# Optimization experiments

Measured on AMD Instinct MI355X. Metric: run time of the kernel, lower is better.

## Reference

```python
import jax, jax.numpy as jnp
import numpy as np

D = 64       # hidden_dim
ED = 16      # edge_dim
N = 50000
E = 400000
T = 2
STEP = 0.5   # euler fixed step over t in [0,1] -> 2 steps
EPS = 1e-5

def setup_inputs() -> dict:
    key = jax.random.key(0)
    ks = jax.random.split(key, 14)
    def lin(k, fi, fo):
        return jax.random.normal(k, (fi, fo), jnp.float32) / np.sqrt(fi)
    return {
        'h_seq': jax.random.normal(ks[0], (T, N, D), jnp.float32),
        'edge_attr': jax.random.normal(ks[1], (T, E, ED), jnp.float32),
        # msg_net: MLP(2D+ED -> D -> D), 2 layers with ReLU
        'W1': lin(ks[2], 2 * D + ED, D), 'b1': jnp.zeros((D,), jnp.float32),
        'W2': lin(ks[3], D, D),          'b2': jnp.zeros((D,), jnp.float32),
        # dynamics_net: Linear(2D,D) -> LayerNorm -> SiLU -> Linear(D,D) -> Tanh
        'Wd1': lin(ks[4], 2 * D, D), 'bd1': jnp.zeros((D,), jnp.float32),
        'ln_g': jnp.ones((D,), jnp.float32), 'ln_b': jnp.zeros((D,), jnp.float32),
        'Wd2': lin(ks[5], D, D), 'bd2': jnp.zeros((D,), jnp.float32),
        'edge_index': jax.random.randint(ks[6], (T, 2, E), 0, N, jnp.int32),
    }

def _ode_func(h, row, col, ea, W1, b1, W2, b2, Wd1, bd1, ln_g, ln_b, Wd2, bd2):
    # identity transport: Q_uv @ h_v == h_v
    h_transported = h[col]                              # [E, D]
    msg_in = jnp.concatenate([h[row], h_transported, ea], axis=-1)  # [E, 2D+ED]
    msg = jax.nn.relu(msg_in @ W1 + b1) @ W2 + b2       # [E, D]
    agg = jax.ops.segment_sum(msg, row, num_segments=h.shape[0])    # [N, D]
    x = jnp.concatenate([h, agg], axis=-1) @ Wd1 + bd1  # [N, D]
    mu = x.mean(-1, keepdims=True)
    var = x.var(-1, keepdims=True)
    x = (x - mu) * jax.lax.rsqrt(var + EPS) * ln_g + ln_b
    x = jax.nn.silu(x) @ Wd2 + bd2
    return jnp.tanh(x)

def reference(h_seq, edge_attr, W1, b1, W2, b2, Wd1, bd1, ln_g, ln_b, Wd2, bd2, edge_index):
    params = (W1, b1, W2, b2, Wd1, bd1, ln_g, ln_b, Wd2, bd2)
    n_steps = int(round(1.0 / STEP))
    h_prev = h_seq[0]
    disagreements = []
    for t in range(T):
        row, col = edge_index[t, 0], edge_index[t, 1]
        ea = edge_attr[t]
        h = h_prev + h_seq[t]                           # h_fused
        for _ in range(n_steps):                        # fixed-step Euler
            h = h + STEP * _ode_func(h, row, col, ea, *params)
        diff = h[row] - h[col]                          # Q=I -> h_u - h_v
        disagreements.append(jnp.minimum((diff * diff).sum(-1), 1e4))
        h_prev = h
    return h_prev, jnp.stack(disagreements)             # h_final [N,D], D [T,E]
```

## Files before the change

kernel.cpp:

```cpp
#include <hip/hip_runtime.h>

#define NN 50000
#define EE 400000
#define NT64 6250
#define EGRID 1250
#define NBLK 782
#define SBLK 49

typedef __bf16 bf16x8 __attribute__((ext_vector_type(8)));
typedef float f32x4 __attribute__((ext_vector_type(4)));

static __device__ __forceinline__ ushort f2bf(float f) {
    union { float f; unsigned int i; } x; x.f = f;
    unsigned int r = x.i + 0x7fffu + ((x.i >> 16) & 1u);
    return (ushort)(r >> 16);
}
static __device__ __forceinline__ float bf2f(ushort u) {
    union { unsigned int i; float f; } x; x.i = ((unsigned int)u) << 16; return x.f;
}
static __device__ __forceinline__ unsigned pack2(float lo, float hi) {
    return (unsigned)f2bf(lo) | ((unsigned)f2bf(hi) << 16);
}
static __device__ __forceinline__ float fast_tanh(float x) {
    float e = __expf(2.f * x);
    return 1.f - 2.f / (e + 1.f);
}
static __device__ __forceinline__ bf16x8 pk8(float4 f0, float4 f1) {
    union { uint4 u; bf16x8 v; } z;
    z.u = make_uint4(pack2(f0.x, f0.y), pack2(f0.z, f0.w),
                     pack2(f1.x, f1.y), pack2(f1.z, f1.w));
    return z.v;
}
static __device__ __forceinline__ bf16x8 zero8() {
    union { uint4 u; bf16x8 v; } z;
    z.u = make_uint4(0u, 0u, 0u, 0u);
    return z.v;
}

__global__ __launch_bounds__(256) void prep_edge_k(
    const float* __restrict__ W1, const float* __restrict__ W2,
    const float* __restrict__ b1, const float* __restrict__ b2,
    ushort* __restrict__ B1P, ushort* __restrict__ B2P,
    float* __restrict__ b1f, float* __restrict__ b2f)
{
    int idx = blockIdx.x * 256 + threadIdx.x;
    if (idx < 10240) {
        int j = idx & 7, n = (idx >> 3) & 63, qk = idx >> 9;
        int kc = qk >> 2, quad = qk & 3;
        int k = kc * 32 + quad * 8 + j;
        B1P[idx] = (k < 144) ? f2bf(W1[k * 64 + n]) : (ushort)0;
    }
    if (idx < 4096) {
        int j = idx & 7, n = (idx >> 3) & 63, qk = idx >> 9;
        int kc = qk >> 2, quad = qk & 3;
        int k = kc * 32 + quad * 8 + j;
        B2P[idx] = f2bf(W2[k * 64 + n]);
    }
    if (idx < 64) { b1f[idx] = b1[idx]; b2f[idx] = b2[idx]; }
}

__global__ __launch_bounds__(256) void prep_node_k(
    const float* __restrict__ Wd1, const float* __restrict__ Wd2,
    const float* __restrict__ bd1, const float* __restrict__ lng,
    const float* __restrict__ lnb, const float* __restrict__ bd2,
    ushort* __restrict__ Wd1P, ushort* __restrict__ Wd2P,
    float* __restrict__ bd1f, float* __restrict__ lngf,
    float* __restrict__ lnbf, float* __restrict__ bd2f)
{
    int idx = blockIdx.x * 256 + threadIdx.x;
    if (idx < 8192) {
        int j = idx & 7, n = (idx >> 3) & 63, qk = idx >> 9;
        int kc = qk >> 2, quad = qk & 3;
        int k = kc * 32 + quad * 8 + j;
        Wd1P[idx] = f2bf(Wd1[k * 64 + n]);
    }
    if (idx < 4096) {
        int j = idx & 7, n = (idx >> 3) & 63, qk = idx >> 9;
        int kc = qk >> 2, quad = qk & 3;
        int k = kc * 32 + quad * 8 + j;
        Wd2P[idx] = f2bf(Wd2[k * 64 + n]);
    }
    if (idx < 64) {
        bd1f[idx] = bd1[idx]; lngf[idx] = lng[idx];
        lnbf[idx] = lnb[idx]; bd2f[idx] = bd2[idx];
    }
}

__global__ __launch_bounds__(256) void state_k(
    float* __restrict__ h, ushort* __restrict__ hb,
    const float* __restrict__ hseq_t, int mode)
{
    int i = blockIdx.x * 256 + threadIdx.x;
    float v = hseq_t[i];
    float r = (mode == 0) ? (2.f * v) : (h[i] + v);
    h[i] = r; hb[i] = f2bf(r);
}

__global__ __launch_bounds__(256) void zero_k(int* __restrict__ p, int n) {
    int i = blockIdx.x * 256 + threadIdx.x;
    if (i < n) p[i] = 0;
}
__global__ __launch_bounds__(256) void zero_f(float* __restrict__ p) {
    int i = blockIdx.x * 256 + threadIdx.x;
    p[i] = 0.f;
}
__global__ __launch_bounds__(256) void hist_k(const int* __restrict__ rows, int* __restrict__ counts) {
    int e = blockIdx.x * 256 + threadIdx.x;
    if (e < EE) atomicAdd(&counts[rows[e]], 1);
}

__global__ __launch_bounds__(256) void scanA_k(
    const int* __restrict__ counts, int* __restrict__ offsets, int* __restrict__ bsum)
{
    __shared__ int wsum[4];
    int tid = threadIdx.x, lane = tid & 63, w = tid >> 6;
    int i4 = blockIdx.x * 1024 + tid * 4;
    int4 v = make_int4(0, 0, 0, 0);
    if (i4 + 3 < NN) v = *(const int4*)(counts + i4);
    else {
        if (i4 < NN) v.x = counts[i4];
        if (i4 + 1 < NN) v.y = counts[i4 + 1];
        if (i4 + 2 < NN) v.z = counts[i4 + 2];
    }
    int s = v.x + v.y + v.z + v.w;
    int x = s;
    for (int off = 1; off < 64; off <<= 1) {
        int y = __shfl_up(x, off);
        if (lane >= off) x += y;
    }
    if (lane == 63) wsum[w] = x;
    __syncthreads();
    int wpre = 0;
    for (int j = 0; j < w; j++) wpre += wsum[j];
    int excl = wpre + x - s;
    int e0 = excl, e1 = e0 + v.x, e2 = e1 + v.y, e3 = e2 + v.z;
    if (i4 + 3 < NN) *(int4*)(offsets + i4) = make_int4(e0, e1, e2, e3);
    else {
        if (i4 < NN) offsets[i4] = e0;
        if (i4 + 1 < NN) offsets[i4 + 1] = e1;
        if (i4 + 2 < NN) offsets[i4 + 2] = e2;
    }
    if (tid == 255) bsum[blockIdx.x] = wpre + x;
}
__global__ __launch_bounds__(64) void scanB_k(const int* __restrict__ bsum, int* __restrict__ bpre) {
    int lane = threadIdx.x;
    int v = (lane < SBLK) ? bsum[lane] : 0;
    int x = v;
    for (int off = 1; off < 64; off <<= 1) {
        int y = __shfl_up(x, off);
        if (lane >= off) x += y;
    }
    if (lane < SBLK) bpre[lane] = x - v;
}
__global__ __launch_bounds__(256) void scanC_k(
    int* __restrict__ offsets, int* __restrict__ cursor, const int* __restrict__ bpre)
{
    int i = blockIdx.x * 256 + threadIdx.x;
    if (i < NN) {
        int o = offsets[i] + bpre[i >> 10];
        offsets[i] = o; cursor[i] = o;
    }
    if (i == 0) offsets[NN] = EE;
}

__global__ __launch_bounds__(256) void fill_k(
    const int* __restrict__ rows, const int* __restrict__ cols,
    const float* __restrict__ ea, int* __restrict__ cursor,
    int* __restrict__ rsort, int* __restrict__ csort, ushort* __restrict__ eab)
{
    int e = blockIdx.x * 256 + threadIdx.x;
    if (e < EE) {
        int r = rows[e];
        int p = atomicAdd(&cursor[r], 1);
        if ((unsigned)p < (unsigned)EE) {
            rsort[p] = r; csort[p] = cols[e];
            const float* sp = ea + (size_t)e * 16;
            float4 f0 = ((const float4*)sp)[0], f1 = ((const float4*)sp)[1];
            float4 f2 = ((const float4*)sp)[2], f3 = ((const float4*)sp)[3];
            uint4* dp = (uint4*)(eab + (size_t)p * 16);
            dp[0] = make_uint4(pack2(f0.x, f0.y), pack2(f0.z, f0.w),
                               pack2(f1.x, f1.y), pack2(f1.z, f1.w));
            dp[1] = make_uint4(pack2(f2.x, f2.y), pack2(f2.z, f2.w),
                               pack2(f3.x, f3.y), pack2(f3.z, f3.w));
        }
    }
}

template<int MODE>
__global__ __launch_bounds__(256, 5) void edge_k(
    const ushort* __restrict__ hb,
    const int* __restrict__ ridx, const int* __restrict__ cidx,
    const ushort* __restrict__ eab, const float* __restrict__ eaf,
    const ushort* __restrict__ B1P, const ushort* __restrict__ B2P,
    const float* __restrict__ b1f, const float* __restrict__ b2f,
    ushort* __restrict__ msg, float* __restrict__ agg)
{
    __shared__ __attribute__((aligned(16))) ushort sB1[10240];
    __shared__ __attribute__((aligned(16))) ushort sH[64 * 72];

    int tid = threadIdx.x;
    int lane = tid & 63, wave = tid >> 6;
    int m = lane & 15, quad = lane >> 4;

    for (int i = tid; i < 10240 / 8; i += 256) ((uint4*)sB1)[i] = ((const uint4*)B1P)[i];
    bf16x8 b2r[2][4];
    for (int kc = 0; kc < 2; kc++)
        for (int nt = 0; nt < 4; nt++)
            b2r[kc][nt] = *(const bf16x8*)(B2P + ((kc * 4 + quad) * 64 + nt * 16 + m) * 8);
    float b1v[4], b2v[4];
    for (int nt = 0; nt < 4; nt++) { b1v[nt] = b1f[nt * 16 + m]; b2v[nt] = b2f[nt * 16 + m]; }
    __syncthreads();

    ushort* sHw = sH + wave * 1152;
    int sl = wave * 16 + m;

    int spf = blockIdx.x * 64 + sl;
    int r_n = ridx[spf], c_n = cidx[spf];

    for (int t = blockIdx.x; t < NT64; t += EGRID) {
        int s = t * 64 + sl;
        int r = r_n, c = c_n;

        bf16x8 a[5];
        a[0] = *(const bf16x8*)(hb + (size_t)r * 64 + quad * 8);
        a[1] = *(const bf16x8*)(hb + (size_t)r * 64 + 32 + quad * 8);
        a[2] = *(const bf16x8*)(hb + (size_t)c * 64 + quad * 8);
        a[3] = *(const bf16x8*)(hb + (size_t)c * 64 + 32 + quad * 8);
        a[4] = zero8();
        if (MODE == 0) {
            if (quad < 2) a[4] = *(const bf16x8*)(eab + (size_t)s * 16 + quad * 8);
        } else {
            if (quad < 2) {
                const float* sp = eaf + (size_t)s * 16 + quad * 8;
                float4 f0 = ((const float4*)sp)[0], f1 = ((const float4*)sp)[1];
                a[4] = pk8(f0, f1);
            }
        }

        int tn = t + EGRID; if (tn >= NT64) tn = t;
        int sn = tn * 64 + sl;
        r_n = ridx[sn]; c_n = cidx[sn];

        f32x4 acc[4];
        #pragma unroll
        for (int nt = 0; nt < 4; nt++) acc[nt] = (f32x4){0.f, 0.f, 0.f, 0.f};
        #pragma unroll
        for (int kc = 0; kc < 5; kc++) {
            #pragma unroll
            for (int nt = 0; nt < 4; nt++) {
                bf16x8 b = *(const bf16x8*)(sB1 + ((kc * 4 + quad) * 64 + nt * 16 + m) * 8);
                acc[nt] = __builtin_amdgcn_mfma_f32_16x16x32_bf16(a[kc], b, acc[nt], 0, 0, 0);
            }
        }

        __builtin_amdgcn_wave_barrier();
        #pragma unroll
        for (int nt = 0; nt < 4; nt++) {
            int colid = nt * 16 + m;
            float bb = b1v[nt];
            #pragma unroll
            for (int rr = 0; rr < 4; rr++) {
                float v = acc[nt][rr] + bb;
                v = v > 0.f ? v : 0.f;
                sHw[(quad * 4 + rr) * 72 + colid] = f2bf(v);
            }
        }
        __builtin_amdgcn_wave_barrier();

        f32x4 acc2[4];
        #pragma unroll
        for (int nt = 0; nt < 4; nt++) acc2[nt] = (f32x4){0.f, 0.f, 0.f, 0.f};
        #pragma unroll
        for (int kc = 0; kc < 2; kc++) {
            bf16x8 av = *(const bf16x8*)(sHw + m * 72 + kc * 32 + quad * 8);
            #pragma unroll
            for (int nt = 0; nt < 4; nt++) {
                acc2[nt] = __builtin_amdgcn_mfma_f32_16x16x32_bf16(av, b2r[kc][nt], acc2[nt], 0, 0, 0);
            }
        }

        int rr4[4];
        if (MODE == 1) {
            #pragma unroll
            for (int rr = 0; rr < 4; rr++) rr4[rr] = ridx[t * 64 + wave * 16 + quad * 4 + rr];
        }
        #pragma unroll
        for (int nt = 0; nt < 4; nt++) {
            int colid = nt * 16 + m;
            float bb = b2v[nt];
            #pragma unroll
            for (int rr = 0; rr < 4; rr++) {
                float v = acc2[nt][rr] + bb;
                int so = t * 64 + wave * 16 + quad * 4 + rr;
                if (MODE == 0) {
                    msg[(size_t)so * 64 + colid] = f2bf(v);
                } else {
                    atomicAdd(&agg[(size_t)rr4[rr] * 64 + colid], v);
                }
            }
        }
    }
}

__global__ __launch_bounds__(256) void agg_k(
    const ushort* __restrict__ msg, const int* __restrict__ offsets,
    float* __restrict__ agg)
{
    int gw = (blockIdx.x * 256 + threadIdx.x) >> 6;
    int lane = threadIdx.x & 63;
    int beg = offsets[gw], end = offsets[gw + 1];
    beg = beg < 0 ? 0 : beg;
    end = end > EE ? EE : end;
    float a = 0.f;
    int i = beg;
    for (; i + 4 <= end; i += 4) {
        a += bf2f(msg[(size_t)i * 64 + lane]);
        a += bf2f(msg[(size_t)(i + 1) * 64 + lane]);
        a += bf2f(msg[(size_t)(i + 2) * 64 + lane]);
        a += bf2f(msg[(size_t)(i + 3) * 64 + lane]);
    }
    for (; i < end; i++) a += bf2f(msg[(size_t)i * 64 + lane]);
    agg[(size_t)gw * 64 + lane] = a;
}

__global__ __launch_bounds__(256, 4) void node_k(
    float* __restrict__ h, ushort* __restrict__ hbm,
    const float* __restrict__ agg,
    const ushort* __restrict__ Wd1P, const ushort* __restrict__ Wd2P,
    const float* __restrict__ bd1f, const float* __restrict__ lngf,
    const float* __restrict__ lnbf, const float* __restrict__ bd2f)
{
    __shared__ __attribute__((aligned(16))) ushort sB1[8192];
    __shared__ __attribute__((aligned(16))) ushort sB2[4096];
    __shared__ __attribute__((aligned(16))) ushort sX[64 * 72];
    int tid = threadIdx.x;
    int lane = tid & 63, wave = tid >> 6;
    int m = lane & 15, quad = lane >> 4;
    int nbase = blockIdx.x * 64;

    for (int i = tid; i < 8192 / 8; i += 256) ((uint4*)sB1)[i] = ((const uint4*)Wd1P)[i];
    for (int i = tid; i < 4096 / 8; i += 256) ((uint4*)sB2)[i] = ((const uint4*)Wd2P)[i];
    float gA[4], bA[4], d1[4], d2[4];
    for (int nt = 0; nt < 4; nt++) {
        int f = nt * 16 + m;
        d1[nt] = bd1f[f]; gA[nt] = lngf[f]; bA[nt] = lnbf[f]; d2[nt] = bd2f[f];
    }
    __syncthreads();

    int n = nbase + wave * 16 + m;
    if (n > NN - 1) n = NN - 1;
    bf16x8 A[4];
    A[0] = *(const bf16x8*)(hbm + (size_t)n * 64 + quad * 8);
    A[1] = *(const bf16x8*)(hbm + (size_t)n * 64 + 32 + quad * 8);
    {
        const float* ap = agg + (size_t)n * 64 + quad * 8;
        A[2] = pk8(((const float4*)ap)[0], ((const float4*)ap)[1]);
        const float* ap2 = agg + (size_t)n * 64 + 32 + quad * 8;
        A[3] = pk8(((const float4*)ap2)[0], ((const float4*)ap2)[1]);
    }

    f32x4 acc[4];
    #pragma unroll
    for (int nt = 0; nt < 4; nt++) acc[nt] = (f32x4){0.f, 0.f, 0.f, 0.f};
    #pragma unroll
    for (int kc = 0; kc < 4; kc++) {
        #pragma unroll
        for (int nt = 0; nt < 4; nt++) {
            bf16x8 b = *(const bf16x8*)(sB1 + ((kc * 4 + quad) * 64 + nt * 16 + m) * 8);
            acc[nt] = __builtin_amdgcn_mfma_f32_16x16x32_bf16(A[kc], b, acc[nt], 0, 0, 0);
        }
    }

    float xs[4][4];
    #pragma unroll
    for (int nt = 0; nt < 4; nt++)
        #pragma unroll
        for (int r = 0; r < 4; r++)
            xs[nt][r] = acc[nt][r] + d1[nt];

    ushort* sXw = sX + wave * 1152;
    #pragma unroll
    for (int r = 0; r < 4; r++) {
        float s1 = 0.f, s2 = 0.f;
        #pragma unroll
        for (int nt = 0; nt < 4; nt++) { float v = xs[nt][r]; s1 += v; s2 += v * v; }
        for (int off = 1; off < 16; off <<= 1) {
            s1 += __shfl_xor(s1, off);
            s2 += __shfl_xor(s2, off);
        }
        float mean = s1 * (1.f / 64.f);
        float var = fmaxf(s2 * (1.f / 64.f) - mean * mean, 0.f);
        float rstd = rsqrtf(var + 1e-5f);
        #pragma unroll
        for (int nt = 0; nt < 4; nt++) {
            float xn = (xs[nt][r] - mean) * rstd * gA[nt] + bA[nt];
            float sl = xn / (1.f + __expf(-xn));
            sXw[(quad * 4 + r) * 72 + nt * 16 + m] = f2bf(sl);
        }
    }
    __builtin_amdgcn_wave_barrier();

    f32x4 acc2[4];
    #pragma unroll
    for (int nt = 0; nt < 4; nt++) acc2[nt] = (f32x4){0.f, 0.f, 0.f, 0.f};
    #pragma unroll
    for (int kc = 0; kc < 2; kc++) {
        bf16x8 av = *(const bf16x8*)(sXw + m * 72 + kc * 32 + quad * 8);
        #pragma unroll
        for (int nt = 0; nt < 4; nt++) {
            bf16x8 b = *(const bf16x8*)(sB2 + ((kc * 4 + quad) * 64 + nt * 16 + m) * 8);
            acc2[nt] = __builtin_amdgcn_mfma_f32_16x16x32_bf16(av, b, acc2[nt], 0, 0, 0);
        }
    }

    #pragma unroll
    for (int r = 0; r < 4; r++) {
        int g = nbase + wave * 16 + quad * 4 + r;
        if (g < NN) {
            #pragma unroll
            for (int nt = 0; nt < 4; nt++) {
                int f = nt * 16 + m;
                float y = fast_tanh(acc2[nt][r] + d2[nt]);
                float hn = h[(size_t)g * 64 + f] + 0.5f * y;
                h[(size_t)g * 64 + f] = hn;
                hbm[(size_t)g * 64 + f] = f2bf(hn);
            }
        }
    }
}

__global__ __launch_bounds__(256) void dis_k(
    const float* __restrict__ h, const int* __restrict__ rows,
    const int* __restrict__ cols, float* __restrict__ outp)
{
    int tid = threadIdx.x;
    int e = blockIdx.x * 16 + (tid >> 4);
    int l16 = tid & 15;
    int r = rows[e], c = cols[e];
    float4 a = *(const float4*)(h + (size_t)r * 64 + l16 * 4);
    float4 b = *(const float4*)(h + (size_t)c * 64 + l16 * 4);
    float dx = a.x - b.x, dy = a.y - b.y, dz = a.z - b.z, dw = a.w - b.w;
    float s = dx * dx + dy * dy + dz * dz + dw * dw;
    for (int off = 1; off < 16; off <<= 1) s += __shfl_xor(s, off);
    if (l16 == 0) outp[e] = (s < 1e4f ? s : 1e4f);
}

__global__ __launch_bounds__(256) void final_k(const float* __restrict__ h, float* __restrict__ out) {
    int i = blockIdx.x * 256 + threadIdx.x;
    out[i] = h[i];
}

extern "C" void kernel_launch(void* const* d_in, const int* in_sizes, int n_in,
                              void* d_out, int out_size, void* d_ws, size_t ws_size,
                              hipStream_t stream) {
    const float* h_seq = (const float*)d_in[0];
    const float* eattr = (const float*)d_in[1];
    const float* W1 = (const float*)d_in[2];
    const float* b1 = (const float*)d_in[3];
    const float* W2 = (const float*)d_in[4];
    const float* b2 = (const float*)d_in[5];
    const float* Wd1 = (const float*)d_in[6];
    const float* bd1 = (const float*)d_in[7];
    const float* lng = (const float*)d_in[8];
    const float* lnb = (const float*)d_in[9];
    const float* Wd2 = (const float*)d_in[10];
    const float* bd2 = (const float*)d_in[11];
    const int* ei = (const int*)d_in[12];
    float* out = (float*)d_out;

    char* wsp = (char*)d_ws;
    size_t used = 0;
    auto carve = [&](size_t b) {
        void* p = (void*)(wsp + used);
        used += (b + 255) & ~(size_t)255;
        return p;
    };
    float* h      = (float*)carve((size_t)NN * 64 * 4);
    ushort* hb    = (ushort*)carve((size_t)NN * 64 * 2);
    float* agg    = (float*)carve((size_t)NN * 64 * 4);
    ushort* B1P   = (ushort*)carve(10240 * 2);
    ushort* B2P   = (ushort*)carve(4096 * 2);
    ushort* Wd1P  = (ushort*)carve(8192 * 2);
    ushort* Wd2P  = (ushort*)carve(4096 * 2);
    float* b1f    = (float*)carve(256);
    float* b2f    = (float*)carve(256);
    float* bd1f   = (float*)carve(256);
    float* lngf   = (float*)carve(256);
    float* lnbf   = (float*)carve(256);
    float* bd2f   = (float*)carve(256);
    int* counts   = (int*)carve((size_t)NN * 4);
    int* offsets  = (int*)carve((size_t)(NN + 1) * 4);
    int* cursor   = (int*)carve((size_t)NN * 4);
    int* bsum     = (int*)carve(256);
    int* bpre     = (int*)carve(256);
    int* rsort    = (int*)carve((size_t)EE * 4);
    int* csort    = (int*)carve((size_t)EE * 4);
    ushort* eab   = (ushort*)carve((size_t)EE * 16 * 2);
    ushort* msg   = (ushort*)carve((size_t)EE * 64 * 2);
    const bool full = (used <= ws_size);

    prep_edge_k<<<40, 256, 0, stream>>>(W1, W2, b1, b2, B1P, B2P, b1f, b2f);
    prep_node_k<<<32, 256, 0, stream>>>(Wd1, Wd2, bd1, lng, lnb, bd2, Wd1P, Wd2P, bd1f, lngf, lnbf, bd2f);

    for (int t = 0; t < 2; t++) {
        const int* rows = ei + (size_t)t * 2 * EE;
        const int* cols = rows + EE;
        const float* eat = eattr + (size_t)t * EE * 16;
        state_k<<<12500, 256, 0, stream>>>(h, hb, h_seq + (size_t)t * NN * 64, t);
        if (full) {
            zero_k<<<196, 256, 0, stream>>>(counts, NN);
            hist_k<<<1563, 256, 0, stream>>>(rows, counts);
            scanA_k<<<SBLK, 256, 0, stream>>>(counts, offsets, bsum);
            scanB_k<<<1, 64, 0, stream>>>(bsum, bpre);
            scanC_k<<<196, 256, 0, stream>>>(offsets, cursor, bpre);
            fill_k<<<1563, 256, 0, stream>>>(rows, cols, eat, cursor, rsort, csort, eab);
        }
        for (int s = 0; s < 2; s++) {
            if (full) {
                edge_k<0><<<EGRID, 256, 0, stream>>>(hb, rsort, csort, eab, (const float*)0,
                                                     B1P, B2P, b1f, b2f, msg, agg);
                agg_k<<<12500, 256, 0, stream>>>(msg, offsets, agg);
            } else {
                zero_f<<<12500, 256, 0, stream>>>(agg);
                edge_k<1><<<EGRID, 256, 0, stream>>>(hb, rows, cols, (const ushort*)0, eat,
                                                     B1P, B2P, b1f, b2f, msg, agg);
            }
            node_k<<<NBLK, 256, 0, stream>>>(h, hb, agg, Wd1P, Wd2P,
                                             bd1f, lngf, lnbf, bd2f);
        }
        dis_k<<<25000, 256, 0, stream>>>(h, rows, cols, out + (size_t)NN * 64 + (size_t)t * EE);
    }
    final_k<<<12500, 256, 0, stream>>>(h, out);
}
```

Before: 542.6 us.

## Fuse segment-sum into edge kernel via run-combined atomics and drop msg buffer

Removes the bf16 per-edge message buffer and the separate CSR aggregation kernel. The edge kernel now adds its outputs straight into the fp32 agg array with atomics, first summing runs of equal consecutive rows, which the row-sorted edge order makes common. The node kernel zeroes agg after reading it, so a memset is only needed once. The sort also changes: scanB is folded into scanC, and fill now scatters only edge ids, with a separate gather kernel that permutes rows, cols and attributes. Edge tiles become contiguous per block (5 tiles each). The cost is atomic contention on high-degree nodes and an extra pass over the edge ids.

```diff
diff --git a/kernel.cpp b/kernel.cpp
--- a/kernel.cpp
+++ b/kernel.cpp
@@ -142,47 +142,46 @@
     }
     if (tid == 255) bsum[blockIdx.x] = wpre + x;
 }
-__global__ __launch_bounds__(64) void scanB_k(const int* __restrict__ bsum, int* __restrict__ bpre) {
-    int lane = threadIdx.x;
-    int v = (lane < SBLK) ? bsum[lane] : 0;
-    int x = v;
-    for (int off = 1; off < 64; off <<= 1) {
-        int y = __shfl_up(x, off);
-        if (lane >= off) x += y;
-    }
-    if (lane < SBLK) bpre[lane] = x - v;
-}
 __global__ __launch_bounds__(256) void scanC_k(
-    int* __restrict__ offsets, int* __restrict__ cursor, const int* __restrict__ bpre)
+    const int* __restrict__ offsets, const int* __restrict__ bsum, int* __restrict__ cursor)
 {
     int i = blockIdx.x * 256 + threadIdx.x;
     if (i < NN) {
-        int o = offsets[i] + bpre[i >> 10];
-        offsets[i] = o; cursor[i] = o;
-    }
-    if (i == 0) offsets[NN] = EE;
-}
-
-__global__ __launch_bounds__(256) void fill_k(
-    const int* __restrict__ rows, const int* __restrict__ cols,
-    const float* __restrict__ ea, int* __restrict__ cursor,
-    int* __restrict__ rsort, int* __restrict__ csort, ushort* __restrict__ eab)
+        int b = i >> 10;
+        int add = 0;
+        for (int j = 0; j < b; j++) add += bsum[j];
+        cursor[i] = offsets[i] + add;
+    }
+}
+
+__global__ __launch_bounds__(256) void fill_idx_k(
+    const int* __restrict__ rows, int* __restrict__ cursor, int* __restrict__ esort)
 {
     int e = blockIdx.x * 256 + threadIdx.x;
     if (e < EE) {
-        int r = rows[e];
-        int p = atomicAdd(&cursor[r], 1);
-        if ((unsigned)p < (unsigned)EE) {
-            rsort[p] = r; csort[p] = cols[e];
-            const float* sp = ea + (size_t)e * 16;
-            float4 f0 = ((const float4*)sp)[0], f1 = ((const float4*)sp)[1];
-            float4 f2 = ((const float4*)sp)[2], f3 = ((const float4*)sp)[3];
-            uint4* dp = (uint4*)(eab + (size_t)p * 16);
-            dp[0] = make_uint4(pack2(f0.x, f0.y), pack2(f0.z, f0.w),
-                               pack2(f1.x, f1.y), pack2(f1.z, f1.w));
-            dp[1] = make_uint4(pack2(f2.x, f2.y), pack2(f2.z, f2.w),
-                               pack2(f3.x, f3.y), pack2(f3.z, f3.w));
-        }
+        int p = atomicAdd(&cursor[rows[e]], 1);
+        if ((unsigned)p < (unsigned)EE) esort[p] = e;
+    }
+}
+
+__global__ __launch_bounds__(256) void gather_k(
+    const int* __restrict__ esort, const int* __restrict__ rows,
+    const int* __restrict__ cols, const float* __restrict__ ea,
+    int* __restrict__ rsort, int* __restrict__ csort, ushort* __restrict__ eab)
+{
+    int p = blockIdx.x * 256 + threadIdx.x;
+    if (p < EE) {
+        int e = esort[p];
+        rsort[p] = rows[e];
+        csort[p] = cols[e];
+        const float* sp = ea + (size_t)e * 16;
+        float4 f0 = ((const float4*)sp)[0], f1 = ((const float4*)sp)[1];
+        float4 f2 = ((const float4*)sp)[2], f3 = ((const float4*)sp)[3];
+        uint4* dp = (uint4*)(eab + (size_t)p * 16);
+        dp[0] = make_uint4(pack2(f0.x, f0.y), pack2(f0.z, f0.w),
+                           pack2(f1.x, f1.y), pack2(f1.z, f1.w));
+        dp[1] = make_uint4(pack2(f2.x, f2.y), pack2(f2.z, f2.w),
+                           pack2(f3.x, f3.y), pack2(f3.z, f3.w));
     }
 }
 
@@ -193,7 +192,7 @@
     const ushort* __restrict__ eab, const float* __restrict__ eaf,
     const ushort* __restrict__ B1P, const ushort* __restrict__ B2P,
     const float* __restrict__ b1f, const float* __restrict__ b2f,
-    ushort* __restrict__ msg, float* __restrict__ agg)
+    float* __restrict__ agg)
 {
     __shared__ __attribute__((aligned(16))) ushort sB1[10240];
     __shared__ __attribute__((aligned(16))) ushort sH[64 * 72];
@@ -214,10 +213,10 @@
     ushort* sHw = sH + wave * 1152;
     int sl = wave * 16 + m;
 
-    int spf = blockIdx.x * 64 + sl;
-    int r_n = ridx[spf], c_n = cidx[spf];
-
-    for (int t = blockIdx.x; t < NT64; t += EGRID) {
+    int t0 = blockIdx.x * 5;
+    int r_n = ridx[t0 * 64 + sl], c_n = cidx[t0 * 64 + sl];
+
+    for (int t = t0; t < t0 + 5; t++) {
         int s = t * 64 + sl;
         int r = r_n, c = c_n;
 
@@ -237,7 +236,7 @@
             }
         }
 
-        int tn = t + EGRID; if (tn >= NT64) tn = t;
+        int tn = t + 1; if (tn >= t0 + 5) tn = t;
         int sn = tn * 64 + sl;
         r_n = ridx[sn]; c_n = cidx[sn];
 
@@ -279,53 +278,29 @@
             }
         }
 
-        int rr4[4];
-        if (MODE == 1) {
-            #pragma unroll
-            for (int rr = 0; rr < 4; rr++) rr4[rr] = ridx[t * 64 + wave * 16 + quad * 4 + rr];
-        }
+        int base = t * 64 + wave * 16 + quad * 4;
+        int r0 = ridx[base], r1 = ridx[base + 1], r2 = ridx[base + 2], r3 = ridx[base + 3];
         #pragma unroll
         for (int nt = 0; nt < 4; nt++) {
             int colid = nt * 16 + m;
             float bb = b2v[nt];
-            #pragma unroll
-            for (int rr = 0; rr < 4; rr++) {
-                float v = acc2[nt][rr] + bb;
-                int so = t * 64 + wave * 16 + quad * 4 + rr;
-                if (MODE == 0) {
-                    msg[(size_t)so * 64 + colid] = f2bf(v);
-                } else {
-                    atomicAdd(&agg[(size_t)rr4[rr] * 64 + colid], v);
-                }
-            }
-        }
-    }
-}
-
-__global__ __launch_bounds__(256) void agg_k(
-    const ushort* __restrict__ msg, const int* __restrict__ offsets,
-    float* __restrict__ agg)
-{
-    int gw = (blockIdx.x * 256 + threadIdx.x) >> 6;
-    int lane = threadIdx.x & 63;
-    int beg = offsets[gw], end = offsets[gw + 1];
-    beg = beg < 0 ? 0 : beg;
-    end = end > EE ? EE : end;
-    float a = 0.f;
-    int i = beg;
-    for (; i + 4 <= end; i += 4) {
-        a += bf2f(msg[(size_t)i * 64 + lane]);
-        a += bf2f(msg[(size_t)(i + 1) * 64 + lane]);
-        a += bf2f(msg[(size_t)(i + 2) * 64 + lane]);
-        a += bf2f(msg[(size_t)(i + 3) * 64 + lane]);
-    }
-    for (; i < end; i++) a += bf2f(msg[(size_t)i * 64 + lane]);
-    agg[(size_t)gw * 64 + lane] = a;
+            float v0 = acc2[nt][0] + bb, v1 = acc2[nt][1] + bb;
+            float v2 = acc2[nt][2] + bb, v3 = acc2[nt][3] + bb;
+            float sum = v0; int pr = r0;
+            if (r1 == pr) sum += v1;
+            else { atomicAdd(&agg[(size_t)pr * 64 + colid], sum); pr = r1; sum = v1; }
+            if (r2 == pr) sum += v2;
+            else { atomicAdd(&agg[(size_t)pr * 64 + colid], sum); pr = r2; sum = v2; }
+            if (r3 == pr) sum += v3;
+            else { atomicAdd(&agg[(size_t)pr * 64 + colid], sum); pr = r3; sum = v3; }
+            atomicAdd(&agg[(size_t)pr * 64 + colid], sum);
+        }
+    }
 }
 
 __global__ __launch_bounds__(256, 4) void node_k(
     float* __restrict__ h, ushort* __restrict__ hbm,
-    const float* __restrict__ agg,
+    float* __restrict__ agg,
     const ushort* __restrict__ Wd1P, const ushort* __restrict__ Wd2P,
     const float* __restrict__ bd1f, const float* __restrict__ lngf,
     const float* __restrict__ lnbf, const float* __restrict__ bd2f)
@@ -347,16 +322,26 @@
     }
     __syncthreads();
 
-    int n = nbase + wave * 16 + m;
-    if (n > NN - 1) n = NN - 1;
+    int n_true = nbase + wave * 16 + m;
+    bool own = (n_true < NN);
+    int n = own ? n_true : (NN - 1);
     bf16x8 A[4];
     A[0] = *(const bf16x8*)(hbm + (size_t)n * 64 + quad * 8);
     A[1] = *(const bf16x8*)(hbm + (size_t)n * 64 + 32 + quad * 8);
     {
         const float* ap = agg + (size_t)n * 64 + quad * 8;
-        A[2] = pk8(((const float4*)ap)[0], ((const float4*)ap)[1]);
+        float4 g0 = ((const float4*)ap)[0], g1 = ((const float4*)ap)[1];
         const float* ap2 = agg + (size_t)n * 64 + 32 + quad * 8;
-        A[3] = pk8(((const float4*)ap2)[0], ((const float4*)ap2)[1]);
+        float4 g2 = ((const float4*)ap2)[0], g3 = ((const float4*)ap2)[1];
+        A[2] = pk8(g0, g1);
+        A[3] = pk8(g2, g3);
+        if (own) {
+            float4 z = make_float4(0.f, 0.f, 0.f, 0.f);
+            ((float4*)(agg + (size_t)n * 64 + quad * 8))[0] = z;
+            ((float4*)(agg + (size_t)n * 64 + quad * 8))[1] = z;
+            ((float4*)(agg + (size_t)n * 64 + 32 + quad * 8))[0] = z;
+            ((float4*)(agg + (size_t)n * 64 + 32 + quad * 8))[1] = z;
+        }
     }
 
     f32x4 acc[4];
@@ -492,13 +477,13 @@
     int* offsets  = (int*)carve((size_t)(NN + 1) * 4);
     int* cursor   = (int*)carve((size_t)NN * 4);
     int* bsum     = (int*)carve(256);
-    int* bpre     = (int*)carve(256);
+    int* esort    = (int*)carve((size_t)EE * 4);
     int* rsort    = (int*)carve((size_t)EE * 4);
     int* csort    = (int*)carve((size_t)EE * 4);
     ushort* eab   = (ushort*)carve((size_t)EE * 16 * 2);
-    ushort* msg   = (ushort*)carve((size_t)EE * 64 * 2);
     const bool full = (used <= ws_size);
 
+    zero_f<<<12500, 256, 0, stream>>>(agg);
     prep_edge_k<<<40, 256, 0, stream>>>(W1, W2, b1, b2, B1P, B2P, b1f, b2f);
     prep_node_k<<<32, 256, 0, stream>>>(Wd1, Wd2, bd1, lng, lnb, bd2, Wd1P, Wd2P, bd1f, lngf, lnbf, bd2f);
 
@@ -511,19 +496,17 @@
             zero_k<<<196, 256, 0, stream>>>(counts, NN);
             hist_k<<<1563, 256, 0, stream>>>(rows, counts);
             scanA_k<<<SBLK, 256, 0, stream>>>(counts, offsets, bsum);
-            scanB_k<<<1, 64, 0, stream>>>(bsum, bpre);
-            scanC_k<<<196, 256, 0, stream>>>(offsets, cursor, bpre);
-            fill_k<<<1563, 256, 0, stream>>>(rows, cols, eat, cursor, rsort, csort, eab);
+            scanC_k<<<196, 256, 0, stream>>>(offsets, bsum, cursor);
+            fill_idx_k<<<1563, 256, 0, stream>>>(rows, cursor, esort);
+            gather_k<<<1563, 256, 0, stream>>>(esort, rows, cols, eat, rsort, csort, eab);
         }
         for (int s = 0; s < 2; s++) {
             if (full) {
                 edge_k<0><<<EGRID, 256, 0, stream>>>(hb, rsort, csort, eab, (const float*)0,
-                                                     B1P, B2P, b1f, b2f, msg, agg);
-                agg_k<<<12500, 256, 0, stream>>>(msg, offsets, agg);
+                                                     B1P, B2P, b1f, b2f, agg);
             } else {
-                zero_f<<<12500, 256, 0, stream>>>(agg);
                 edge_k<1><<<EGRID, 256, 0, stream>>>(hb, rows, cols, (const ushort*)0, eat,
-                                                     B1P, B2P, b1f, b2f, msg, agg);
+                                                     B1P, B2P, b1f, b2f, agg);
             }
             node_k<<<NBLK, 256, 0, stream>>>(h, hb, agg, Wd1P, Wd2P,
                                              bd1f, lngf, lnbf, bd2f);
```

New measurement: 659.1 us. +21.5%, slower.

## Split CSR fill into index scatter plus coalesced gather; contiguous edge tiles per block

Applied to the files above, without the earlier changes.

The atomic-based fill kernel now scatters only the edge id into a sorted permutation. A separate gather kernel then writes rsort, csort and the bf16 edge attributes with coalesced writes in sorted order, instead of scattering 32-byte attribute rows. The edge kernel now gives each block five consecutive 64-edge tiles rather than a grid-strided set, which may improve locality of the row-sorted h gathers. The fallback path gets a node kernel that zeroes agg after reading it, removing a per-step zero pass, at the cost of an extra kernel launch and esort buffer on the main path.

```diff
diff --git a/kernel.cpp b/kernel.cpp
--- a/kernel.cpp
+++ b/kernel.cpp
@@ -163,26 +163,34 @@
     if (i == 0) offsets[NN] = EE;
 }
 
-__global__ __launch_bounds__(256) void fill_k(
-    const int* __restrict__ rows, const int* __restrict__ cols,
-    const float* __restrict__ ea, int* __restrict__ cursor,
-    int* __restrict__ rsort, int* __restrict__ csort, ushort* __restrict__ eab)
+__global__ __launch_bounds__(256) void fill_idx_k(
+    const int* __restrict__ rows, int* __restrict__ cursor, int* __restrict__ esort)
 {
     int e = blockIdx.x * 256 + threadIdx.x;
     if (e < EE) {
-        int r = rows[e];
-        int p = atomicAdd(&cursor[r], 1);
-        if ((unsigned)p < (unsigned)EE) {
-            rsort[p] = r; csort[p] = cols[e];
-            const float* sp = ea + (size_t)e * 16;
-            float4 f0 = ((const float4*)sp)[0], f1 = ((const float4*)sp)[1];
-            float4 f2 = ((const float4*)sp)[2], f3 = ((const float4*)sp)[3];
-            uint4* dp = (uint4*)(eab + (size_t)p * 16);
-            dp[0] = make_uint4(pack2(f0.x, f0.y), pack2(f0.z, f0.w),
-                               pack2(f1.x, f1.y), pack2(f1.z, f1.w));
-            dp[1] = make_uint4(pack2(f2.x, f2.y), pack2(f2.z, f2.w),
-                               pack2(f3.x, f3.y), pack2(f3.z, f3.w));
-        }
+        int p = atomicAdd(&cursor[rows[e]], 1);
+        if ((unsigned)p < (unsigned)EE) esort[p] = e;
+    }
+}
+
+__global__ __launch_bounds__(256) void gather_k(
+    const int* __restrict__ esort, const int* __restrict__ rows,
+    const int* __restrict__ cols, const float* __restrict__ ea,
+    int* __restrict__ rsort, int* __restrict__ csort, ushort* __restrict__ eab)
+{
+    int p = blockIdx.x * 256 + threadIdx.x;
+    if (p < EE) {
+        int e = esort[p];
+        rsort[p] = rows[e];
+        csort[p] = cols[e];
+        const float* sp = ea + (size_t)e * 16;
+        float4 f0 = ((const float4*)sp)[0], f1 = ((const float4*)sp)[1];
+        float4 f2 = ((const float4*)sp)[2], f3 = ((const float4*)sp)[3];
+        uint4* dp = (uint4*)(eab + (size_t)p * 16);
+        dp[0] = make_uint4(pack2(f0.x, f0.y), pack2(f0.z, f0.w),
+                           pack2(f1.x, f1.y), pack2(f1.z, f1.w));
+        dp[1] = make_uint4(pack2(f2.x, f2.y), pack2(f2.z, f2.w),
+                           pack2(f3.x, f3.y), pack2(f3.z, f3.w));
     }
 }
 
@@ -214,10 +222,10 @@
     ushort* sHw = sH + wave * 1152;
     int sl = wave * 16 + m;
 
-    int spf = blockIdx.x * 64 + sl;
-    int r_n = ridx[spf], c_n = cidx[spf];
-
-    for (int t = blockIdx.x; t < NT64; t += EGRID) {
+    int t0 = blockIdx.x * 5;
+    int r_n = ridx[t0 * 64 + sl], c_n = cidx[t0 * 64 + sl];
+
+    for (int t = t0; t < t0 + 5; t++) {
         int s = t * 64 + sl;
         int r = r_n, c = c_n;
 
@@ -237,7 +245,7 @@
             }
         }
 
-        int tn = t + EGRID; if (tn >= NT64) tn = t;
+        int tn = t + 1; if (tn >= t0 + 5) tn = t;
         int sn = tn * 64 + sl;
         r_n = ridx[sn]; c_n = cidx[sn];
 
@@ -347,16 +355,19 @@
     }
     __syncthreads();
 
-    int n = nbase + wave * 16 + m;
-    if (n > NN - 1) n = NN - 1;
+    int n_true = nbase + wave * 16 + m;
+    bool own = (n_true < NN);
+    int n = own ? n_true : (NN - 1);
     bf16x8 A[4];
     A[0] = *(const bf16x8*)(hbm + (size_t)n * 64 + quad * 8);
     A[1] = *(const bf16x8*)(hbm + (size_t)n * 64 + 32 + quad * 8);
     {
         const float* ap = agg + (size_t)n * 64 + quad * 8;
-        A[2] = pk8(((const float4*)ap)[0], ((const float4*)ap)[1]);
+        float4 g0 = ((const float4*)ap)[0], g1 = ((const float4*)ap)[1];
         const float* ap2 = agg + (size_t)n * 64 + 32 + quad * 8;
-        A[3] = pk8(((const float4*)ap2)[0], ((const float4*)ap2)[1]);
+        float4 g2 = ((const float4*)ap2)[0], g3 = ((const float4*)ap2)[1];
+        A[2] = pk8(g0, g1);
+        A[3] = pk8(g2, g3);
     }
 
     f32x4 acc[4];
@@ -370,6 +381,121 @@
             acc[nt] = __builtin_amdgcn_mfma_f32_16x16x32_bf16(A[kc], b, acc[nt], 0, 0, 0);
         }
     }
+
+    float xs[4][4];
+    #pragma unroll
+    for (int nt = 0; nt < 4; nt++)
+        #pragma unroll
+        for (int r = 0; r < 4; r++)
+            xs[nt][r] = acc[nt][r] + d1[nt];
+
+    ushort* sXw = sX + wave * 1152;
+    #pragma unroll
+    for (int r = 0; r < 4; r++) {
+        float s1 = 0.f, s2 = 0.f;
+        #pragma unroll
+        for (int nt = 0; nt < 4; nt++) { float v = xs[nt][r]; s1 += v; s2 += v * v; }
+        for (int off = 1; off < 16; off <<= 1) {
+            s1 += __shfl_xor(s1, off);
+            s2 += __shfl_xor(s2, off);
+        }
+        float mean = s1 * (1.f / 64.f);
+        float var = fmaxf(s2 * (1.f / 64.f) - mean * mean, 0.f);
+        float rstd = rsqrtf(var + 1e-5f);
+        #pragma unroll
+        for (int nt = 0; nt < 4; nt++) {
+            float xn = (xs[nt][r] - mean) * rstd * gA[nt] + bA[nt];
+            float sl = xn / (1.f + __expf(-xn));
+            sXw[(quad * 4 + r) * 72 + nt * 16 + m] = f2bf(sl);
+        }
+    }
+    __builtin_amdgcn_wave_barrier();
+
+    f32x4 acc2[4];
+    #pragma unroll
+    for (int nt = 0; nt < 4; nt++) acc2[nt] = (f32x4){0.f, 0.f, 0.f, 0.f};
+    #pragma unroll
+    for (int kc = 0; kc < 2; kc++) {
+        bf16x8 av = *(const bf16x8*)(sXw + m * 72 + kc * 32 + quad * 8);
+        #pragma unroll
+        for (int nt = 0; nt < 4; nt++) {
+            bf16x8 b = *(const bf16x8*)(sB2 + ((kc * 4 + quad) * 64 + nt * 16 + m) * 8);
+            acc2[nt] = __builtin_amdgcn_mfma_f32_16x16x32_bf16(av, b, acc2[nt], 0, 0, 0);
+        }
+    }
+
+    #pragma unroll
+    for (int r = 0; r < 4; r++) {
+        int g = nbase + wave * 16 + quad * 4 + r;
+        if (g < NN) {
+            #pragma unroll
+            for (int nt = 0; nt < 4; nt++) {
+                int f = nt * 16 + m;
+                float y = fast_tanh(acc2[nt][r] + d2[nt]);
+                float hn = h[(size_t)g * 64 + f] + 0.5f * y;
+                h[(size_t)g * 64 + f] = hn;
+                hbm[(size_t)g * 64 + f] = f2bf(hn);
+            }
+        }
+    }
+}
+
+__global__ __launch_bounds__(256, 4) void node_fb_k(
+    float* __restrict__ h, ushort* __restrict__ hbm,
+    float* __restrict__ agg,
+    const ushort* __restrict__ Wd1P, const ushort* __restrict__ Wd2P,
+    const float* __restrict__ bd1f, const float* __restrict__ lngf,
+    const float* __restrict__ lnbf, const float* __restrict__ bd2f)
+{
+    __shared__ __attribute__((aligned(16))) ushort sB1[8192];
+    __shared__ __attribute__((aligned(16))) ushort sB2[4096];
+    __shared__ __attribute__((aligned(16))) ushort sX[64 * 72];
+    int tid = threadIdx.x;
+    int lane = tid & 63, wave = tid >> 6;
+    int m = lane & 15, quad = lane >> 4;
+    int nbase = blockIdx.x * 64;
+
+    for (int i = tid; i < 8192 / 8; i += 256) ((uint4*)sB1)[i] = ((const uint4*)Wd1P)[i];
+    for (int i = tid; i < 4096 / 8; i += 256) ((uint4*)sB2)[i] = ((const uint4*)Wd2P)[i];
+    float gA[4], bA[4], d1[4], d2[4];
+    for (int nt = 0; nt < 4; nt++) {
+        int f = nt * 16 + m;
+        d1[nt] = bd1f[f]; gA[nt] = lngf[f]; bA[nt] = lnbf[f]; d2[nt] = bd2f[f];
+    }
+    __syncthreads();
+
+    int n_true = nbase + wave * 16 + m;
+    bool own = (n_true < NN);
+    int n = own ? n_true : (NN - 1);
+    bf16x8 A[4];
+    A[0] = *(const bf16x8*)(hbm + (size_t)n * 64 + quad * 8);
+    A[1] = *(const bf16x8*)(hbm + (size_t)n * 64 + 32 + quad * 8);
+    {
+        const float* ap = agg + (size_t)n * 64 + quad * 8;
+        float4 g0 = ((const float4*)ap)[0], g1 = ((const float4*)ap)[1];
+        const float* ap2 = agg + (size_t)n * 64 + 32 + quad * 8;
+        float4 g2 = ((const float4*)ap2)[0], g3 = ((const float4*)ap2)[1];
+        A[2] = pk8(g0, g1);
+        A[3] = pk8(g2, g3);
+        if (own) {
+            float4 z = make_float4(0.f, 0.f, 0.f, 0.f);
+            ((float4*)(agg + (size_t)n * 64 + quad * 8))[0] = z;
+            ((float4*)(agg + (size_t)n * 64 + quad * 8))[1] = z;
+            ((float4*)(agg + (size_t)n * 64 + 32 + quad * 8))[0] = z;
+            ((float4*)(agg + (size_t)n * 64 + 32 + quad * 8))[1] = z;
+        }
+    }
+
+    f32x4 acc[4];
+    #pragma unroll
+    for (int nt = 0; nt < 4; nt++) acc[nt] = (f32x4){0.f, 0.f, 0.f, 0.f};
+    #pragma unroll
+    for (int kc = 0; kc < 4; kc++)
+        #pragma unroll
+        for (int nt = 0; nt < 4; nt++) {
+            bf16x8 b = *(const bf16x8*)(sB1 + ((kc * 4 + quad) * 64 + nt * 16 + m) * 8);
+            acc[nt] = __builtin_amdgcn_mfma_f32_16x16x32_bf16(A[kc], b, acc[nt], 0, 0, 0);
+        }
 
     float xs[4][4];
     #pragma unroll
@@ -493,6 +619,7 @@
     int* cursor   = (int*)carve((size_t)NN * 4);
     int* bsum     = (int*)carve(256);
     int* bpre     = (int*)carve(256);
+    int* esort    = (int*)carve((size_t)EE * 4);
     int* rsort    = (int*)carve((size_t)EE * 4);
     int* csort    = (int*)carve((size_t)EE * 4);
     ushort* eab   = (ushort*)carve((size_t)EE * 16 * 2);
@@ -501,6 +628,7 @@
 
     prep_edge_k<<<40, 256, 0, stream>>>(W1, W2, b1, b2, B1P, B2P, b1f, b2f);
     prep_node_k<<<32, 256, 0, stream>>>(Wd1, Wd2, bd1, lng, lnb, bd2, Wd1P, Wd2P, bd1f, lngf, lnbf, bd2f);
+    if (!full) zero_f<<<12500, 256, 0, stream>>>(agg);
 
     for (int t = 0; t < 2; t++) {
         const int* rows = ei + (size_t)t * 2 * EE;
@@ -513,20 +641,22 @@
             scanA_k<<<SBLK, 256, 0, stream>>>(counts, offsets, bsum);
             scanB_k<<<1, 64, 0, stream>>>(bsum, bpre);
             scanC_k<<<196, 256, 0, stream>>>(offsets, cursor, bpre);
-            fill_k<<<1563, 256, 0, stream>>>(rows, cols, eat, cursor, rsort, csort, eab);
+            fill_idx_k<<<1563, 256, 0, stream>>>(rows, cursor, esort);
+            gather_k<<<1563, 256, 0, stream>>>(esort, rows, cols, eat, rsort, csort, eab);
         }
         for (int s = 0; s < 2; s++) {
             if (full) {
                 edge_k<0><<<EGRID, 256, 0, stream>>>(hb, rsort, csort, eab, (const float*)0,
                                                      B1P, B2P, b1f, b2f, msg, agg);
                 agg_k<<<12500, 256, 0, stream>>>(msg, offsets, agg);
+                node_k<<<NBLK, 256, 0, stream>>>(h, hb, agg, Wd1P, Wd2P,
+                                                 bd1f, lngf, lnbf, bd2f);
             } else {
-                zero_f<<<12500, 256, 0, stream>>>(agg);
                 edge_k<1><<<EGRID, 256, 0, stream>>>(hb, rows, cols, (const ushort*)0, eat,
                                                      B1P, B2P, b1f, b2f, msg, agg);
-            }
-            node_k<<<NBLK, 256, 0, stream>>>(h, hb, agg, Wd1P, Wd2P,
-                                             bd1f, lngf, lnbf, bd2f);
+                node_fb_k<<<NBLK, 256, 0, stream>>>(h, hb, agg, Wd1P, Wd2P,
+                                                    bd1f, lngf, lnbf, bd2f);
+            }
         }
         dis_k<<<25000, 256, 0, stream>>>(h, rows, cols, out + (size_t)NN * 64 + (size_t)t * EE);
     }
```

Result: no change. 545.0 us (+0.4%).
